# Performance work log

Measured on AMD Instinct MI355X. Metric: run time of the kernel, lower is better.

## Reference

```python
import jax, jax.numpy as jnp
import numpy as np
from jax import lax

K = 3          # kernel_size
STRIDE = 2
BN_EPS = 1e-5
CLAMP_MIN = 1e-4


def setup_inputs() -> dict:
    key = jax.random.key(0)
    k1, k2 = jax.random.split(key)
    x = jax.random.normal(k1, (16, 64, 112, 112), dtype=jnp.float32)
    # kaiming-normal fan_out init: std = sqrt(2 / (out_ch * kh * kw))
    std = np.sqrt(2.0 / (9 * 3 * 3)).astype(np.float32)
    conv_w = jax.random.normal(k2, (9, 64, 3, 3), dtype=jnp.float32) * std
    gamma = jnp.ones((9,), dtype=jnp.float32)
    beta = jnp.zeros((9,), dtype=jnp.float32)
    return {"x": x, "conv_w": conv_w, "gamma": gamma, "beta": beta}


def reference(x, conv_w, gamma, beta):
    p = K // 2
    n, c, h, w = x.shape
    xp = jnp.pad(x, ((0, 0), (0, 0), (p, p), (p, p)), mode="reflect")  # [n,c,h+2p,w+2p]

    # sigma = BN(conv(pad(x))) with 3x3 conv, stride 1, no bias -> [n, k*k, h, w]
    sigma = lax.conv_general_dilated(
        xp, conv_w, window_strides=(1, 1), padding="VALID",
        dimension_numbers=("NCHW", "OIHW", "NCHW"))
    mean = jnp.mean(sigma, axis=(0, 2, 3), keepdims=True)
    var = jnp.var(sigma, axis=(0, 2, 3), keepdims=True)
    sigma = (sigma - mean) * lax.rsqrt(var + BN_EPS)
    sigma = sigma * gamma[None, :, None, None] + beta[None, :, None, None]
    sigma = jnp.clip(sigma, CLAMP_MIN)               # clamp(min=1e-4)
    sigma = sigma / jnp.sum(sigma, axis=1, keepdims=True)  # normalize over k*k taps

    # unfold pad(x) into k*k patches -> [n, c*k*k, h, w] (channel-major like torch unfold)
    patches = lax.conv_general_dilated_patches(
        xp, filter_shape=(K, K), window_strides=(1, 1), padding="VALID",
        dimension_numbers=("NCHW", "OIHW", "NCHW"))
    patches = patches.reshape(n, c, K * K, h, w)

    out = jnp.sum(patches * sigma[:, None], axis=2)  # [n, c, h, w]
    return out[:, :, ::STRIDE, ::STRIDE]
```

## Files before the change

kernel.cpp:

```cpp
#include <hip/hip_runtime.h>
#include <math.h>

namespace {

constexpr int Hh = 112, Ww = 112, Cc = 64, Nn = 16;
constexpr int OHh = 56, OWw = 56;
constexpr int HW = Hh * Ww;
constexpr int OP = OHh * OWw;
constexpr int NP = Nn * OP;
constexpr int NHW = Nn * HW;
constexpr float BN_EPS_F = 1e-5f;
constexpr float CLAMP_MIN_F = 1e-4f;
constexpr int NSTAT = 32;
constexpr int CH = 32;

__global__ __launch_bounds__(256) void conv_half_kernel(
    const float* __restrict__ x, const float* __restrict__ wgt,
    float* __restrict__ P)
{
    const int tid = threadIdx.x;
    const int b = blockIdx.x;
    const int swz = (b & 7) * 98 + (b >> 3);
    const int half = swz / 392;
    const int bid = swz - half * 392;

    const int s = bid * 256 + tid;
    const int pos0 = 2 * s;
    const int n = pos0 / HW;
    const int hw = pos0 - n * HW;
    const int h = hw / Ww;
    const int w0 = hw - h * Ww;

    const int hm = (h == 0) ? 1 : h - 1;
    const int hp = (h == Hh - 1) ? (Hh - 2) : (h + 1);
    const int wl = (w0 == 0) ? 1 : w0 - 1;
    const int wr = (w0 == Ww - 2) ? (Ww - 2) : (w0 + 2);

    const int ro[3] = { hm * Ww, h * Ww, hp * Ww };

    const float* xb = x + ((size_t)n * Cc + half * CH) * HW;

    float m0[3], m1[3], el[3], er[3];
    float n_m0[3], n_m1[3], n_el[3], n_er[3];
#pragma unroll
    for (int r = 0; r < 3; ++r) {
        const float2 f2 = *(const float2*)(xb + ro[r] + w0);
        m0[r] = f2.x; m1[r] = f2.y;
        el[r] = xb[ro[r] + wl];
        er[r] = xb[ro[r] + wr];
    }

    float acc0[9], acc1[9];
#pragma unroll
    for (int k = 0; k < 9; ++k) { acc0[k] = 0.f; acc1[k] = 0.f; }

#pragma unroll 2
    for (int c = 0; c < CH; ++c) {
        const float* xn = xb + (size_t)((c + 1) & (CH - 1)) * HW;
#pragma unroll
        for (int r = 0; r < 3; ++r) {
            const float2 f2 = *(const float2*)(xn + ro[r] + w0);
            n_m0[r] = f2.x; n_m1[r] = f2.y;
            n_el[r] = xn[ro[r] + wl];
            n_er[r] = xn[ro[r] + wr];
        }

        const int cg = half * CH + c;
#pragma unroll
        for (int k = 0; k < 9; ++k) {
            const float* wk = wgt + ((size_t)k * Cc + cg) * 9;
#pragma unroll
            for (int r = 0; r < 3; ++r) {
                const float wa = wk[3 * r], wb = wk[3 * r + 1], wc = wk[3 * r + 2];
                acc0[k] = fmaf(wa, el[r], acc0[k]);
                acc0[k] = fmaf(wb, m0[r], acc0[k]);
                acc0[k] = fmaf(wc, m1[r], acc0[k]);
                acc1[k] = fmaf(wa, m0[r], acc1[k]);
                acc1[k] = fmaf(wb, m1[r], acc1[k]);
                acc1[k] = fmaf(wc, er[r], acc1[k]);
            }
        }

#pragma unroll
        for (int r = 0; r < 3; ++r) {
            m0[r] = n_m0[r]; m1[r] = n_m1[r];
            el[r] = n_el[r]; er[r] = n_er[r];
        }
    }

    float* Ph = P + (size_t)half * 9 * NHW;
#pragma unroll
    for (int k = 0; k < 9; ++k)
        *(float2*)(Ph + (size_t)k * NHW + pos0) = make_float2(acc0[k], acc1[k]);
}

__global__ __launch_bounds__(256) void merge_stats_kernel(
    const float* __restrict__ P, double* __restrict__ stats,
    float* __restrict__ sig_even )
{
    __shared__ float rs[4], rq[4];
    const int tid = threadIdx.x;
    const int k = blockIdx.y;
    const int p = blockIdx.x * 256 + tid;

    const float v = P[(size_t)k * NHW + p] + P[(size_t)(9 + k) * NHW + p];

    const int w = p % Ww;
    const int h = (p / Ww) % Hh;
    const int n = p / HW;
    if (!(w & 1) && !(h & 1))
        sig_even[(size_t)k * NP + n * OP + (h >> 1) * OWw + (w >> 1)] = v;

    float s = v, q = v * v;
#pragma unroll
    for (int off = 32; off > 0; off >>= 1) {
        s += __shfl_down(s, off, 64);
        q += __shfl_down(q, off, 64);
    }
    const int lane = tid & 63, wv = tid >> 6;
    if (lane == 0) { rs[wv] = s; rq[wv] = q; }
    __syncthreads();
    if (tid == 0) {
        double* st = stats + (size_t)(blockIdx.x & (NSTAT - 1)) * 18;
        atomicAdd(&st[k], (double)(rs[0] + rs[1] + rs[2] + rs[3]));
        atomicAdd(&st[9 + k], (double)(rq[0] + rq[1] + rq[2] + rq[3]));
    }
}

__global__ __launch_bounds__(256) void apply_kernel(
    const float* __restrict__ x, const float* __restrict__ sig_raw,
    const float* __restrict__ gamma, const float* __restrict__ beta,
    const double* __restrict__ stats, float* __restrict__ out)
{
    __shared__ float srow[9][OWw];
    __shared__ float mean_s[9], istd_s[9], gb[18];

    const int tid = threadIdx.x;
    const int f = blockIdx.x;
    const int fs = (f & 7) * 112 + (f >> 3);
    const int n = fs / OHh;
    const int oh = fs % OHh;

    if (tid < 9) {
        double s = 0.0, q = 0.0;
        for (int r = 0; r < NSTAT; ++r) { s += stats[r * 18 + tid]; q += stats[r * 18 + 9 + tid]; }
        const double cnt = (double)Nn * HW;
        const double m = s / cnt;
        const double v = q / cnt - m * m;
        mean_s[tid] = (float)m;
        istd_s[tid] = (float)(1.0 / sqrt(v + (double)BN_EPS_F));
        gb[tid] = gamma[tid];
        gb[9 + tid] = beta[tid];
    }
    __syncthreads();

    if (tid < OWw) {
        const int pp = n * OP + oh * OWw + tid;
        float s[9], ssum = 0.f;
#pragma unroll
        for (int k = 0; k < 9; ++k) {
            float v = fmaf((sig_raw[(size_t)k * NP + pp] - mean_s[k]) * istd_s[k], gb[k], gb[9 + k]);
            v = fmaxf(v, CLAMP_MIN_F);
            s[k] = v;
            ssum += v;
        }
        const float inv = 1.f / ssum;
#pragma unroll
        for (int k = 0; k < 9; ++k) srow[k][tid] = s[k] * inv;
    }
    __syncthreads();

    const int csub = tid >> 6;
    const int lane = tid & 63;
    if (lane >= OWw) return;
    const int ow = lane;

    const int r0 = (oh == 0) ? 1 : (2 * oh - 1);
    const int r1 = 2 * oh, r2 = 2 * oh + 1;
    const int c0 = (ow == 0) ? 1 : (2 * ow - 1);
    const int c1 = 2 * ow, c2 = 2 * ow + 1;

    float sg[9];
#pragma unroll
    for (int k = 0; k < 9; ++k) sg[k] = srow[k][ow];

#pragma unroll 2
    for (int cc = 0; cc < 16; ++cc) {
        const int c = cc * 4 + csub;
        const float* xc = x + ((size_t)(n * Cc + c)) * HW;
        float o = 0.f;
        o = fmaf(sg[0], xc[r0 * Ww + c0], o);
        o = fmaf(sg[1], xc[r0 * Ww + c1], o);
        o = fmaf(sg[2], xc[r0 * Ww + c2], o);
        o = fmaf(sg[3], xc[r1 * Ww + c0], o);
        o = fmaf(sg[4], xc[r1 * Ww + c1], o);
        o = fmaf(sg[5], xc[r1 * Ww + c2], o);
        o = fmaf(sg[6], xc[r2 * Ww + c0], o);
        o = fmaf(sg[7], xc[r2 * Ww + c1], o);
        o = fmaf(sg[8], xc[r2 * Ww + c2], o);
        out[((size_t)(n * Cc + c)) * OP + oh * OWw + ow] = o;
    }
}

}

extern "C" void kernel_launch(void* const* d_in, const int* in_sizes, int n_in,
                              void* d_out, int out_size, void* d_ws, size_t ws_size,
                              hipStream_t stream) {
    const float* x     = (const float*)d_in[0];
    const float* wgt   = (const float*)d_in[1];
    const float* gamma = (const float*)d_in[2];
    const float* beta  = (const float*)d_in[3];
    float* out = (float*)d_out;

    double* stats = (double*)d_ws;
    float* P        = (float*)((char*)d_ws + 8192);
    float* sig_even = P + (size_t)18 * NHW;

    hipMemsetAsync(d_ws, 0, 8192, stream);
    conv_half_kernel<<<784, 256, 0, stream>>>(x, wgt, P);
    merge_stats_kernel<<<dim3(NHW / 256, 9), 256, 0, stream>>>(P, stats, sig_even);
    apply_kernel<<<896, 256, 0, stream>>>(x, sig_even, gamma, beta, stats, out);
}
```

Measured before the change: 76.03 us.

## Split conv channel reduction four ways and vectorize merge-stats kernel

Measured after the change: 71.42 us. 1.06x faster.

```diff
diff --git a/kernel.cpp b/kernel.cpp
--- a/kernel.cpp
+++ b/kernel.cpp
@@ -12,17 +12,20 @@
 constexpr float BN_EPS_F = 1e-5f;
 constexpr float CLAMP_MIN_F = 1e-4f;
 constexpr int NSTAT = 32;
-constexpr int CH = 32;
-
-__global__ __launch_bounds__(256) void conv_half_kernel(
+
+template <int NSPLIT>
+__global__ __launch_bounds__(256) void conv_split_kernel(
     const float* __restrict__ x, const float* __restrict__ wgt,
-    float* __restrict__ P)
+    float* __restrict__ P )
 {
+    constexpr int CHS = Cc / NSPLIT;
+    constexpr int NBLK = NSPLIT * 392;
+
     const int tid = threadIdx.x;
     const int b = blockIdx.x;
-    const int swz = (b & 7) * 98 + (b >> 3);
-    const int half = swz / 392;
-    const int bid = swz - half * 392;
+    const int swz = (b & 7) * (NBLK / 8) + (b >> 3);
+    const int part = swz / 392;
+    const int bid = swz - part * 392;
 
     const int s = bid * 256 + tid;
     const int pos0 = 2 * s;
@@ -38,7 +41,7 @@
 
     const int ro[3] = { hm * Ww, h * Ww, hp * Ww };
 
-    const float* xb = x + ((size_t)n * Cc + half * CH) * HW;
+    const float* xb = x + ((size_t)n * Cc + part * CHS) * HW;
 
     float m0[3], m1[3], el[3], er[3];
     float n_m0[3], n_m1[3], n_el[3], n_er[3];
@@ -55,8 +58,8 @@
     for (int k = 0; k < 9; ++k) { acc0[k] = 0.f; acc1[k] = 0.f; }
 
 #pragma unroll 2
-    for (int c = 0; c < CH; ++c) {
-        const float* xn = xb + (size_t)((c + 1) & (CH - 1)) * HW;
+    for (int c = 0; c < CHS; ++c) {
+        const float* xn = xb + (size_t)((c + 1) & (CHS - 1)) * HW;
 #pragma unroll
         for (int r = 0; r < 3; ++r) {
             const float2 f2 = *(const float2*)(xn + ro[r] + w0);
@@ -65,7 +68,7 @@
             n_er[r] = xn[ro[r] + wr];
         }
 
-        const int cg = half * CH + c;
+        const int cg = part * CHS + c;
 #pragma unroll
         for (int k = 0; k < 9; ++k) {
             const float* wk = wgt + ((size_t)k * Cc + cg) * 9;
@@ -88,12 +91,13 @@
         }
     }
 
-    float* Ph = P + (size_t)half * 9 * NHW;
+    float* Ph = P + (size_t)part * 9 * NHW;
 #pragma unroll
     for (int k = 0; k < 9; ++k)
         *(float2*)(Ph + (size_t)k * NHW + pos0) = make_float2(acc0[k], acc1[k]);
 }
 
+template <int NSPLIT>
 __global__ __launch_bounds__(256) void merge_stats_kernel(
     const float* __restrict__ P, double* __restrict__ stats,
     float* __restrict__ sig_even )
@@ -101,17 +105,25 @@
     __shared__ float rs[4], rq[4];
     const int tid = threadIdx.x;
     const int k = blockIdx.y;
-    const int p = blockIdx.x * 256 + tid;
-
-    const float v = P[(size_t)k * NHW + p] + P[(size_t)(9 + k) * NHW + p];
-
-    const int w = p % Ww;
-    const int h = (p / Ww) % Hh;
-    const int n = p / HW;
-    if (!(w & 1) && !(h & 1))
-        sig_even[(size_t)k * NP + n * OP + (h >> 1) * OWw + (w >> 1)] = v;
-
-    float s = v, q = v * v;
+    const int p0 = (blockIdx.x * 256 + tid) * 4;
+
+    float4 v = *(const float4*)(P + (size_t)k * NHW + p0);
+#pragma unroll
+    for (int qq = 1; qq < NSPLIT; ++qq) {
+        const float4 t = *(const float4*)(P + ((size_t)qq * 9 + k) * NHW + p0);
+        v.x += t.x; v.y += t.y; v.z += t.z; v.w += t.w;
+    }
+
+    const int w = p0 % Ww;
+    const int h = (p0 / Ww) % Hh;
+    const int n = p0 / HW;
+    if (!(h & 1)) {
+        *(float2*)(sig_even + (size_t)k * NP + n * OP + (h >> 1) * OWw + (w >> 1)) =
+            make_float2(v.x, v.z);
+    }
+
+    float s = v.x + v.y + v.z + v.w;
+    float q = v.x * v.x + v.y * v.y + v.z * v.z + v.w * v.w;
 #pragma unroll
     for (int off = 32; off > 0; off >>= 1) {
         s += __shfl_down(s, off, 64);
@@ -214,11 +226,21 @@
     float* out = (float*)d_out;
 
     double* stats = (double*)d_ws;
-    float* P        = (float*)((char*)d_ws + 8192);
-    float* sig_even = P + (size_t)18 * NHW;
-
+    float* P = (float*)((char*)d_ws + 8192);
+
+    const size_t sig_bytes = (size_t)9 * NP * 4;
+    const size_t need4 = 8192 + (size_t)36 * NHW * 4 + sig_bytes;
     hipMemsetAsync(d_ws, 0, 8192, stream);
-    conv_half_kernel<<<784, 256, 0, stream>>>(x, wgt, P);
-    merge_stats_kernel<<<dim3(NHW / 256, 9), 256, 0, stream>>>(P, stats, sig_even);
-    apply_kernel<<<896, 256, 0, stream>>>(x, sig_even, gamma, beta, stats, out);
-}
+
+    if (ws_size >= need4) {
+        float* sig_even = P + (size_t)36 * NHW;
+        conv_split_kernel<4><<<1568, 256, 0, stream>>>(x, wgt, P);
+        merge_stats_kernel<4><<<dim3(196, 9), 256, 0, stream>>>(P, stats, sig_even);
+        apply_kernel<<<896, 256, 0, stream>>>(x, sig_even, gamma, beta, stats, out);
+    } else {
+        float* sig_even = P + (size_t)18 * NHW;
+        conv_split_kernel<2><<<784, 256, 0, stream>>>(x, wgt, P);
+        merge_stats_kernel<2><<<dim3(196, 9), 256, 0, stream>>>(P, stats, sig_even);
+        apply_kernel<<<896, 256, 0, stream>>>(x, sig_even, gamma, beta, stats, out);
+    }
+}
```
